# Optimization experiments

Hardware: AMD Instinct MI355X
Metric: run time of the kernel (lower is better)

Reference implementation:

```python
import jax, jax.numpy as jnp
import numpy as np

B, N, D, H, E = 4, 1024, 1024, 2048, 8

def setup_inputs() -> dict:
    key = jax.random.key(0)
    ks = jax.random.split(key, 5)
    return {
        "x": jax.random.normal(ks[0], (B, N, D), dtype=jnp.float32),
        "gate_w": jax.random.normal(ks[1], (D, E), dtype=jnp.float32) * 0.02,
        "gate_b": jnp.zeros((E,), dtype=jnp.float32),
        "w1": jax.random.normal(ks[2], (E, D, H), dtype=jnp.float32) * 0.02,
        "b1": jnp.zeros((E, H), dtype=jnp.float32),
        "w2": jax.random.normal(ks[3], (E, H, D), dtype=jnp.float32) * 0.02,
        "b2": jnp.zeros((E, D), dtype=jnp.float32),
        "gamma": jnp.ones((D,), dtype=jnp.float32),
    }

def reference(x, gate_w, gate_b, w1, b1, w2, b2, gamma):
    b, n, d = x.shape
    e = w1.shape[0]
    xf = x.reshape(b * n, d)                                    # [T, D]
    # gate: softmax over experts, then top-1
    probs = jax.nn.softmax(xf @ gate_w + gate_b, axis=-1)       # [T, E]
    top_val = jnp.max(probs, axis=-1, keepdims=True)            # [T, 1]
    top_idx = jnp.argmax(probs, axis=-1)                        # [T]
    # all-expert FFN (dense reference for masked dispatch; dropout in eval)
    h = jax.nn.gelu(jnp.einsum('td,edh->eth', xf, w1) + b1[:, None, :],
                    approximate=False)                          # [E, T, H]
    eo = jnp.einsum('eth,ehd->etd', h, w2) + b2[:, None, :]     # [E, T, D]
    onehot = jax.nn.one_hot(top_idx, e, dtype=xf.dtype)         # [T, E]
    out = jnp.einsum('etd,te->td', eo, onehot)                  # select routed expert
    y = (xf + out * top_val).reshape(b, n, d)
    # RMSNorm: F.normalize (L2, eps=1e-12) * gamma * sqrt(dim)
    nrm = jnp.linalg.norm(y, axis=-1, keepdims=True)
    y = y / jnp.maximum(nrm, 1e-12) * gamma * np.float32(np.sqrt(d))
    # load-balancing loss (unbiased variance like torch.var)
    importance = probs.sum(axis=0)                              # [E]
    load_loss = jnp.var(importance, ddof=1) / (jnp.mean(importance) ** 2 + 1e-10)
    return jax.nn.gelu(y, approximate=False), load_loss
```

## Files before the change

kernel.cpp:

```cpp
#include <hip/hip_runtime.h>
#include <math.h>

#define T_TOK 4096
#define DIM   1024
#define HID   2048
#define NE    8
#define TMM   128
#define TNN   64
#define BK    64

typedef unsigned int  u32;
typedef unsigned short u16;
typedef __attribute__((ext_vector_type(8))) short bf16x8;
typedef __attribute__((ext_vector_type(4))) float f32x4;

__device__ __forceinline__ float gelu_exact(float v) {
    return 0.5f * v * (1.0f + erff(v * 0.70710678118654752440f));
}

__device__ __forceinline__ float gelu_fast(float x) {
    float u = 1.5957691216057308f * (x + 0.044715f * x * x * x);
    float e = __expf(u);
    float t = 1.f - 2.f / (e + 1.f);
    return 0.5f * x * (1.f + t);
}

__device__ __forceinline__ u16 f2bf(float v) {
    u32 u = __float_as_uint(v);
    u32 r = (u + 0x7FFFu + ((u >> 16) & 1u)) >> 16;
    return (u16)r;
}

__device__ __forceinline__ void gld_lds16(const void* g, void* l) {
    __builtin_amdgcn_global_load_lds(
        (const __attribute__((address_space(1))) u32*)g,
        (__attribute__((address_space(3))) u32*)l,
        16, 0, 0);
}

__global__ __launch_bounds__(256) void gate_kernel(
    const float* __restrict__ x, const float* __restrict__ gw,
    const float* __restrict__ gb, float* __restrict__ top_val,
    int* __restrict__ top_idx, float* __restrict__ importance,
    int* __restrict__ counts)
{
    __shared__ float s_imp[NE];
    __shared__ int   s_cnt[NE];
    if (threadIdx.x < NE) { s_imp[threadIdx.x] = 0.f; s_cnt[threadIdx.x] = 0; }
    __syncthreads();

    const int wave = threadIdx.x >> 6;
    const int lane = threadIdx.x & 63;
    const int t = blockIdx.x * 4 + wave;

    float acc[NE];
    #pragma unroll
    for (int e = 0; e < NE; e++) acc[e] = 0.f;

    const float* xr = x + (size_t)t * DIM;
    #pragma unroll 4
    for (int k = lane; k < DIM; k += 64) {
        float xv = xr[k];
        const float* g = gw + (size_t)k * NE;
        float4 g0 = *(const float4*)g;
        float4 g1 = *(const float4*)(g + 4);
        acc[0] += xv * g0.x; acc[1] += xv * g0.y;
        acc[2] += xv * g0.z; acc[3] += xv * g0.w;
        acc[4] += xv * g1.x; acc[5] += xv * g1.y;
        acc[6] += xv * g1.z; acc[7] += xv * g1.w;
    }
    #pragma unroll
    for (int e = 0; e < NE; e++) {
        #pragma unroll
        for (int off = 32; off > 0; off >>= 1)
            acc[e] += __shfl_down(acc[e], off, 64);
    }
    if (lane == 0) {
        float l[NE];
        float m = -1e30f;
        #pragma unroll
        for (int e = 0; e < NE; e++) { l[e] = acc[e] + gb[e]; m = fmaxf(m, l[e]); }
        float s = 0.f;
        #pragma unroll
        for (int e = 0; e < NE; e++) { l[e] = expf(l[e] - m); s += l[e]; }
        float inv = 1.f / s;
        int bi = 0; float bv = -1.f;
        #pragma unroll
        for (int e = 0; e < NE; e++) {
            float p = l[e] * inv;
            atomicAdd(&s_imp[e], p);
            if (p > bv) { bv = p; bi = e; }
        }
        top_val[t] = bv;
        top_idx[t] = bi;
        atomicAdd(&s_cnt[bi], 1);
    }
    __syncthreads();
    if (threadIdx.x < NE) {
        atomicAdd(&importance[threadIdx.x], s_imp[threadIdx.x]);
        atomicAdd(&counts[threadIdx.x],     s_cnt[threadIdx.x]);
    }
}

__global__ void plan_kernel(const int* __restrict__ counts,
                            const float* __restrict__ importance,
                            int* __restrict__ offsets, int* __restrict__ tile_e,
                            int* __restrict__ tile_s, int* __restrict__ tile_rows,
                            int* __restrict__ ntiles, float* __restrict__ loss_out)
{
    if (threadIdx.x == 0 && blockIdx.x == 0) {
        int off = 0, nt = 0;
        for (int e = 0; e < NE; e++) {
            offsets[e] = off;
            int c = counts[e];
            for (int s = 0; s < c; s += TMM) {
                tile_e[nt] = e;
                tile_s[nt] = off + s;
                tile_rows[nt] = min(TMM, c - s);
                nt++;
            }
            off += c;
        }
        offsets[NE] = off;
        *ntiles = nt;

        float mean = 0.f;
        for (int e = 0; e < NE; e++) mean += importance[e];
        mean *= (1.0f / NE);
        float var = 0.f;
        for (int e = 0; e < NE; e++) { float d = importance[e] - mean; var += d * d; }
        var *= (1.0f / (NE - 1));
        loss_out[0] = var / (mean * mean + 1e-10f);
    }
}

__global__ void scatter_kernel(const int* __restrict__ top_idx,
                               const int* __restrict__ offsets,
                               int* __restrict__ cursors,
                               int* __restrict__ sorted_tok)
{
    int t = blockIdx.x * blockDim.x + threadIdx.x;
    if (t < T_TOK) {
        int e = top_idx[t];
        int pos = atomicAdd(&cursors[e], 1);
        sorted_tok[offsets[e] + pos] = t;
    }
}

__global__ __launch_bounds__(256) void gather_x_kernel(
    const float* __restrict__ x, const int* __restrict__ sorted_tok,
    u16* __restrict__ xs)
{
    const int s = blockIdx.x;
    const int tok = sorted_tok[s];
    const float* src = x + (size_t)tok * DIM;
    u16* dst = xs + (size_t)s * DIM;
    const int i = threadIdx.x * 4;
    float4 v = *(const float4*)&src[i];
    ushort4 o;
    o.x = f2bf(v.x); o.y = f2bf(v.y); o.z = f2bf(v.z); o.w = f2bf(v.w);
    *(ushort4*)&dst[i] = o;
}

__global__ __launch_bounds__(256) void transpose_bf16_kernel(
    const float* __restrict__ in, u16* __restrict__ out, int R, int C)
{
    __shared__ float tile[32][33];
    const float* src = in  + (size_t)blockIdx.z * R * C;
    u16*         dst = out + (size_t)blockIdx.z * R * C;
    const int c0 = blockIdx.x * 32, r0 = blockIdx.y * 32;
    const int tc = threadIdx.x & 31, tr = threadIdx.x >> 5;
    #pragma unroll
    for (int i = 0; i < 4; i++) {
        int r = tr + i * 8;
        tile[r][tc] = src[(size_t)(r0 + r) * C + c0 + tc];
    }
    __syncthreads();
    #pragma unroll
    for (int i = 0; i < 4; i++) {
        int cc = tr + i * 8;
        float v = tile[tc][cc];
        dst[(size_t)(c0 + cc) * R + r0 + tc] = f2bf(v);
    }
}

__global__ __launch_bounds__(256) void ffn1_mfma(
    const u16* __restrict__ xs, const u16* __restrict__ w1t,
    const float* __restrict__ b1,
    const int* __restrict__ tile_e, const int* __restrict__ tile_s,
    const int* __restrict__ tile_rows, const int* __restrict__ ntiles,
    u16* __restrict__ h_buf)
{
    const int tile = blockIdx.x;
    if (tile >= *ntiles) return;
    const int e     = tile_e[tile];
    const int sbase = tile_s[tile];
    const int rows  = tile_rows[tile];
    const int nbase = blockIdx.y * TNN;

    __shared__ __align__(16) u16 As[TMM * BK];
    __shared__ __align__(16) u16 Bs[TNN * BK];

    const int th = threadIdx.x;
    const int w  = th >> 6;
    const int l  = th & 63;
    const int wm = w >> 1, wn = w & 1;
    const int lr = l >> 3;
    const int lc = (l & 7) * 8;

    const u16* aptr[4];
    #pragma unroll
    for (int c = 0; c < 4; c++) {
        int srow = sbase + w * 32 + c * 8 + lr;
        if (srow > T_TOK - 1) srow = T_TOK - 1;
        aptr[c] = xs + (size_t)srow * DIM + lc;
    }
    const u16* wb = w1t + (size_t)e * HID * DIM + (size_t)nbase * DIM;
    const u16* bptr[2];
    #pragma unroll
    for (int c = 0; c < 2; c++)
        bptr[c] = wb + (size_t)(w * 16 + c * 8 + lr) * DIM + lc;

    f32x4 acc[4][2] = {};

    for (int k0 = 0; k0 < DIM; k0 += BK) {
        __syncthreads();
        #pragma unroll
        for (int c = 0; c < 4; c++)
            gld_lds16(aptr[c] + k0, &As[(w * 32 + c * 8) * BK]);
        #pragma unroll
        for (int c = 0; c < 2; c++)
            gld_lds16(bptr[c] + k0, &Bs[(w * 16 + c * 8) * BK]);
        __syncthreads();
        #pragma unroll
        for (int ks = 0; ks < 2; ks++) {
            const int ko = ks * 32 + (l >> 4) * 8;
            bf16x8 af[4], bfr[2];
            #pragma unroll
            for (int i = 0; i < 4; i++)
                af[i]  = *(const bf16x8*)&As[(wm * 64 + i * 16 + (l & 15)) * BK + ko];
            #pragma unroll
            for (int i = 0; i < 2; i++)
                bfr[i] = *(const bf16x8*)&Bs[(wn * 32 + i * 16 + (l & 15)) * BK + ko];
            #pragma unroll
            for (int mi = 0; mi < 4; mi++)
                #pragma unroll
                for (int ni = 0; ni < 2; ni++)
                    acc[mi][ni] = __builtin_amdgcn_mfma_f32_16x16x32_bf16(
                        af[mi], bfr[ni], acc[mi][ni], 0, 0, 0);
        }
    }

    const int col = l & 15, quad = l >> 4;
    #pragma unroll
    for (int ni = 0; ni < 2; ni++) {
        const int n = nbase + wn * 32 + ni * 16 + col;
        const float bias = b1[e * HID + n];
        #pragma unroll
        for (int mi = 0; mi < 4; mi++) {
            #pragma unroll
            for (int r = 0; r < 4; r++) {
                const int m = wm * 64 + mi * 16 + quad * 4 + r;
                if (m < rows) {
                    float v = acc[mi][ni][r] + bias;
                    h_buf[(size_t)(sbase + m) * HID + n] = f2bf(gelu_fast(v));
                }
            }
        }
    }
}

__global__ __launch_bounds__(256) void ffn2_mfma(
    const u16* __restrict__ h_buf, const u16* __restrict__ w2t,
    const float* __restrict__ b2, const float* __restrict__ x,
    const int* __restrict__ sorted_tok, const float* __restrict__ top_val,
    const int* __restrict__ tile_e, const int* __restrict__ tile_s,
    const int* __restrict__ tile_rows, const int* __restrict__ ntiles,
    float* __restrict__ yout)
{
    const int tile = blockIdx.x;
    if (tile >= *ntiles) return;
    const int e     = tile_e[tile];
    const int sbase = tile_s[tile];
    const int rows  = tile_rows[tile];
    const int nbase = blockIdx.y * TNN;

    __shared__ __align__(16) u16 As[TMM * BK];
    __shared__ __align__(16) u16 Bs[TNN * BK];

    const int th = threadIdx.x;
    const int w  = th >> 6;
    const int l  = th & 63;
    const int wm = w >> 1, wn = w & 1;
    const int lr = l >> 3;
    const int lc = (l & 7) * 8;

    const u16* aptr[4];
    #pragma unroll
    for (int c = 0; c < 4; c++) {
        int srow = sbase + w * 32 + c * 8 + lr;
        if (srow > T_TOK - 1) srow = T_TOK - 1;
        aptr[c] = h_buf + (size_t)srow * HID + lc;
    }
    const u16* wb = w2t + (size_t)e * DIM * HID + (size_t)nbase * HID;
    const u16* bptr[2];
    #pragma unroll
    for (int c = 0; c < 2; c++)
        bptr[c] = wb + (size_t)(w * 16 + c * 8 + lr) * HID + lc;

    f32x4 acc[4][2] = {};

    for (int k0 = 0; k0 < HID; k0 += BK) {
        __syncthreads();
        #pragma unroll
        for (int c = 0; c < 4; c++)
            gld_lds16(aptr[c] + k0, &As[(w * 32 + c * 8) * BK]);
        #pragma unroll
        for (int c = 0; c < 2; c++)
            gld_lds16(bptr[c] + k0, &Bs[(w * 16 + c * 8) * BK]);
        __syncthreads();
        #pragma unroll
        for (int ks = 0; ks < 2; ks++) {
            const int ko = ks * 32 + (l >> 4) * 8;
            bf16x8 af[4], bfr[2];
            #pragma unroll
            for (int i = 0; i < 4; i++)
                af[i]  = *(const bf16x8*)&As[(wm * 64 + i * 16 + (l & 15)) * BK + ko];
            #pragma unroll
            for (int i = 0; i < 2; i++)
                bfr[i] = *(const bf16x8*)&Bs[(wn * 32 + i * 16 + (l & 15)) * BK + ko];
            #pragma unroll
            for (int mi = 0; mi < 4; mi++)
                #pragma unroll
                for (int ni = 0; ni < 2; ni++)
                    acc[mi][ni] = __builtin_amdgcn_mfma_f32_16x16x32_bf16(
                        af[mi], bfr[ni], acc[mi][ni], 0, 0, 0);
        }
    }

    const int col = l & 15, quad = l >> 4;
    float bias[2];
    #pragma unroll
    for (int ni = 0; ni < 2; ni++)
        bias[ni] = b2[e * DIM + nbase + wn * 32 + ni * 16 + col];

    #pragma unroll
    for (int mi = 0; mi < 4; mi++) {
        #pragma unroll
        for (int r = 0; r < 4; r++) {
            const int m = wm * 64 + mi * 16 + quad * 4 + r;
            if (m < rows) {
                const int t = sorted_tok[sbase + m];
                const float tv = top_val[t];
                #pragma unroll
                for (int ni = 0; ni < 2; ni++) {
                    const int n = nbase + wn * 32 + ni * 16 + col;
                    float v = acc[mi][ni][r] + bias[ni];
                    yout[(size_t)t * DIM + n] = x[(size_t)t * DIM + n] + v * tv;
                }
            }
        }
    }
}

__global__ __launch_bounds__(256) void norm_kernel(float* __restrict__ y,
                                                   const float* __restrict__ gamma)
{
    const int t = blockIdx.x;
    float* row = y + (size_t)t * DIM;
    const int th = threadIdx.x;
    float4 v = *(const float4*)&row[th * 4];
    float ss = v.x * v.x + v.y * v.y + v.z * v.z + v.w * v.w;

    const int lane = th & 63, wave = th >> 6;
    #pragma unroll
    for (int off = 32; off > 0; off >>= 1) ss += __shfl_down(ss, off, 64);
    __shared__ float red[4];
    if (lane == 0) red[wave] = ss;
    __syncthreads();
    float total = red[0] + red[1] + red[2] + red[3];

    float nrm = sqrtf(total);
    float scale = 32.0f / fmaxf(nrm, 1e-12f);

    float4 g = *(const float4*)&gamma[th * 4];
    float4 o;
    o.x = gelu_exact(v.x * scale * g.x);
    o.y = gelu_exact(v.y * scale * g.y);
    o.z = gelu_exact(v.z * scale * g.z);
    o.w = gelu_exact(v.w * scale * g.w);
    *(float4*)&row[th * 4] = o;
}

extern "C" void kernel_launch(void* const* d_in, const int* in_sizes, int n_in,
                              void* d_out, int out_size, void* d_ws, size_t ws_size,
                              hipStream_t stream) {
    const float* x      = (const float*)d_in[0];
    const float* gate_w = (const float*)d_in[1];
    const float* gate_b = (const float*)d_in[2];
    const float* w1     = (const float*)d_in[3];
    const float* b1     = (const float*)d_in[4];
    const float* w2     = (const float*)d_in[5];
    const float* b2     = (const float*)d_in[6];
    const float* gamma  = (const float*)d_in[7];

    float* out  = (float*)d_out;
    float* loss = out + (size_t)T_TOK * DIM;

    char* ws = (char*)d_ws;
    float* top_val    = (float*)(ws + 0);
    int*   top_idx    = (int*)  (ws + 16384);
    int*   sorted_tok = (int*)  (ws + 32768);
    float* importance = (float*)(ws + 49152);
    int*   counts     = (int*)  (ws + 49184);
    int*   cursors    = (int*)  (ws + 49216);
    int*   offsets    = (int*)  (ws + 49248);
    int*   tile_e     = (int*)  (ws + 49536);
    int*   tile_s     = (int*)  (ws + 49824);
    int*   tile_rows  = (int*)  (ws + 50112);
    int*   ntiles     = (int*)  (ws + 50400);
    u16*   x_sorted   = (u16*)  (ws + 65536);
    u16*   h_buf      = (u16*)  (ws + 65536 + 8388608);
    u16*   w1t        = (u16*)  (ws + 65536 + 8388608 + 16777216);
    u16*   w2t        = (u16*)  (ws + 65536 + 8388608 + 16777216 + 33554432);

    hipMemsetAsync(ws + 49152, 0, 96, stream);

    gate_kernel<<<T_TOK / 4, 256, 0, stream>>>(x, gate_w, gate_b, top_val,
                                               top_idx, importance, counts);
    plan_kernel<<<1, 64, 0, stream>>>(counts, importance, offsets, tile_e,
                                      tile_s, tile_rows, ntiles, loss);
    scatter_kernel<<<T_TOK / 256, 256, 0, stream>>>(top_idx, offsets, cursors,
                                                    sorted_tok);
    gather_x_kernel<<<T_TOK, 256, 0, stream>>>(x, sorted_tok, x_sorted);
    transpose_bf16_kernel<<<dim3(HID / 32, DIM / 32, NE), 256, 0, stream>>>(
        w1, w1t, DIM, HID);
    transpose_bf16_kernel<<<dim3(DIM / 32, HID / 32, NE), 256, 0, stream>>>(
        w2, w2t, HID, DIM);

    ffn1_mfma<<<dim3(40, HID / TNN), 256, 0, stream>>>(
        x_sorted, w1t, b1, tile_e, tile_s, tile_rows, ntiles, h_buf);
    ffn2_mfma<<<dim3(40, DIM / TNN), 256, 0, stream>>>(
        h_buf, w2t, b2, x, sorted_tok, top_val, tile_e, tile_s, tile_rows,
        ntiles, out);
    norm_kernel<<<T_TOK, 256, 0, stream>>>(out, gamma);
}
```

Before: 346.8 us.

## Swizzle LDS tiles in expert GEMMs and widen weight transpose to 64x64 vector tiles

Applies an XOR swizzle to the column chunk each lane loads into LDS, with a matching swizzled read offset in the MFMA inner loop of both FFN GEMMs, to avoid LDS bank conflicts on bf16x8 fragment reads. Also rewrites the fp32-to-bf16 weight transpose to use 64x64 tiles with float4 loads and ushort4 stores, so fewer, wider global memory transactions are issued. The swizzle keeps the same data per row, only permuted, so correctness depends on the read and write mappings matching. The padded 64x65 fp32 tile uses more shared memory per block in the transpose.

```diff
diff --git a/kernel.cpp b/kernel.cpp
--- a/kernel.cpp
+++ b/kernel.cpp
@@ -165,22 +165,33 @@
 __global__ __launch_bounds__(256) void transpose_bf16_kernel(
     const float* __restrict__ in, u16* __restrict__ out, int R, int C)
 {
-    __shared__ float tile[32][33];
+    __shared__ float tile[64][65];
     const float* src = in  + (size_t)blockIdx.z * R * C;
     u16*         dst = out + (size_t)blockIdx.z * R * C;
-    const int c0 = blockIdx.x * 32, r0 = blockIdx.y * 32;
-    const int tc = threadIdx.x & 31, tr = threadIdx.x >> 5;
+    const int c0 = blockIdx.x * 64, r0 = blockIdx.y * 64;
+    const int th = threadIdx.x;
+
+    const int tr  = th >> 4;
+    const int tc4 = (th & 15) * 4;
     #pragma unroll
     for (int i = 0; i < 4; i++) {
-        int r = tr + i * 8;
-        tile[r][tc] = src[(size_t)(r0 + r) * C + c0 + tc];
+        const int r = tr + i * 16;
+        float4 v = *(const float4*)&src[(size_t)(r0 + r) * C + c0 + tc4];
+        tile[r][tc4 + 0] = v.x; tile[r][tc4 + 1] = v.y;
+        tile[r][tc4 + 2] = v.z; tile[r][tc4 + 3] = v.w;
     }
     __syncthreads();
+    const int cc  = th >> 4;
+    const int rr4 = (th & 15) * 4;
     #pragma unroll
     for (int i = 0; i < 4; i++) {
-        int cc = tr + i * 8;
-        float v = tile[tc][cc];
-        dst[(size_t)(c0 + cc) * R + r0 + tc] = f2bf(v);
+        const int c = cc + i * 16;
+        ushort4 o;
+        o.x = f2bf(tile[rr4 + 0][c]);
+        o.y = f2bf(tile[rr4 + 1][c]);
+        o.z = f2bf(tile[rr4 + 2][c]);
+        o.w = f2bf(tile[rr4 + 3][c]);
+        *(ushort4*)&dst[(size_t)(c0 + c) * R + r0 + rr4] = o;
     }
 }
 
@@ -206,20 +217,20 @@
     const int l  = th & 63;
     const int wm = w >> 1, wn = w & 1;
     const int lr = l >> 3;
-    const int lc = (l & 7) * 8;
+    const int lcs = ((l & 7) ^ lr) * 8;
 
     const u16* aptr[4];
     #pragma unroll
     for (int c = 0; c < 4; c++) {
         int srow = sbase + w * 32 + c * 8 + lr;
         if (srow > T_TOK - 1) srow = T_TOK - 1;
-        aptr[c] = xs + (size_t)srow * DIM + lc;
+        aptr[c] = xs + (size_t)srow * DIM + lcs;
     }
     const u16* wb = w1t + (size_t)e * HID * DIM + (size_t)nbase * DIM;
     const u16* bptr[2];
     #pragma unroll
     for (int c = 0; c < 2; c++)
-        bptr[c] = wb + (size_t)(w * 16 + c * 8 + lr) * DIM + lc;
+        bptr[c] = wb + (size_t)(w * 16 + c * 8 + lr) * DIM + lcs;
 
     f32x4 acc[4][2] = {};
 
@@ -234,7 +245,7 @@
         __syncthreads();
         #pragma unroll
         for (int ks = 0; ks < 2; ks++) {
-            const int ko = ks * 32 + (l >> 4) * 8;
+            const int ko = ((ks * 4 + (l >> 4)) ^ (l & 7)) * 8;
             bf16x8 af[4], bfr[2];
             #pragma unroll
             for (int i = 0; i < 4; i++)
@@ -293,20 +304,20 @@
     const int l  = th & 63;
     const int wm = w >> 1, wn = w & 1;
     const int lr = l >> 3;
-    const int lc = (l & 7) * 8;
+    const int lcs = ((l & 7) ^ lr) * 8;
 
     const u16* aptr[4];
     #pragma unroll
     for (int c = 0; c < 4; c++) {
         int srow = sbase + w * 32 + c * 8 + lr;
         if (srow > T_TOK - 1) srow = T_TOK - 1;
-        aptr[c] = h_buf + (size_t)srow * HID + lc;
+        aptr[c] = h_buf + (size_t)srow * HID + lcs;
     }
     const u16* wb = w2t + (size_t)e * DIM * HID + (size_t)nbase * HID;
     const u16* bptr[2];
     #pragma unroll
     for (int c = 0; c < 2; c++)
-        bptr[c] = wb + (size_t)(w * 16 + c * 8 + lr) * HID + lc;
+        bptr[c] = wb + (size_t)(w * 16 + c * 8 + lr) * HID + lcs;
 
     f32x4 acc[4][2] = {};
 
@@ -321,7 +332,7 @@
         __syncthreads();
         #pragma unroll
         for (int ks = 0; ks < 2; ks++) {
-            const int ko = ks * 32 + (l >> 4) * 8;
+            const int ko = ((ks * 4 + (l >> 4)) ^ (l & 7)) * 8;
             bf16x8 af[4], bfr[2];
             #pragma unroll
             for (int i = 0; i < 4; i++)
@@ -433,9 +444,9 @@
     scatter_kernel<<<T_TOK / 256, 256, 0, stream>>>(top_idx, offsets, cursors,
                                                     sorted_tok);
     gather_x_kernel<<<T_TOK, 256, 0, stream>>>(x, sorted_tok, x_sorted);
-    transpose_bf16_kernel<<<dim3(HID / 32, DIM / 32, NE), 256, 0, stream>>>(
+    transpose_bf16_kernel<<<dim3(HID / 64, DIM / 64, NE), 256, 0, stream>>>(
         w1, w1t, DIM, HID);
-    transpose_bf16_kernel<<<dim3(DIM / 32, HID / 32, NE), 256, 0, stream>>>(
+    transpose_bf16_kernel<<<dim3(DIM / 64, HID / 64, NE), 256, 0, stream>>>(
         w2, w2t, HID, DIM);
 
     ffn1_mfma<<<dim3(40, HID / TNN), 256, 0, stream>>>(
```

After: 334.6 us. -3.5%, faster.
